# Optimization experiments

Hardware: AMD Instinct MI355X
Metric: run time of the kernel (lower is better)

Reference implementation:

```python
import jax, jax.numpy as jnp
import numpy as np

N_NODES = 50000
N_EDGES = 600000
D = 128
H_MLP = 256
N_LABELS = 10
EPS = 0.0  # tf_geometric GIN default eps


def _gin_layer(x, src, dst, W, b):
    # gather neighbor (source) features and sum-aggregate into destinations
    msg = x[src]                                   # [E, D] irregular gather
    agg = jax.ops.segment_sum(msg, dst, num_segments=N_NODES)  # [N, D]
    h = (1.0 + EPS) * x + agg                      # GIN sum update
    return jax.nn.relu(h @ W + b)                  # dense transform + relu


def setup_inputs() -> dict:
    key = jax.random.key(0)
    ks = jax.random.split(key, 8)
    x = jax.random.normal(ks[0], (N_NODES, D), dtype=jnp.float32)
    edge_index = jax.random.randint(ks[1], (2, N_EDGES), 0, N_NODES, dtype=jnp.int32)
    s = 1.0 / np.sqrt(D)
    W0 = jax.random.normal(ks[2], (D, D), dtype=jnp.float32) * s
    W1 = jax.random.normal(ks[3], (D, D), dtype=jnp.float32) * s
    W2 = jax.random.normal(ks[4], (D, D), dtype=jnp.float32) * s
    Wm1 = jax.random.normal(ks[5], (D, H_MLP), dtype=jnp.float32) * s
    Wm2 = jax.random.normal(ks[6], (H_MLP, N_LABELS), dtype=jnp.float32) * (1.0 / np.sqrt(H_MLP))
    return {
        'x': x, 'edge_index': edge_index,
        'W0': W0, 'b0': jnp.zeros((D,), jnp.float32),
        'W1': W1, 'b1': jnp.zeros((D,), jnp.float32),
        'W2': W2, 'b2': jnp.zeros((D,), jnp.float32),
        'Wm1': Wm1, 'bm1': jnp.zeros((H_MLP,), jnp.float32),
        'Wm2': Wm2, 'bm2': jnp.zeros((N_LABELS,), jnp.float32),
    }


def reference(x, edge_index, W0, b0, W1, b1, W2, b2, Wm1, bm1, Wm2, bm2):
    src, dst = edge_index[0], edge_index[1]
    h = _gin_layer(x, src, dst, W0, b0)
    h = _gin_layer(h, src, dst, W1, b1)
    h = _gin_layer(h, src, dst, W2, b2)
    # head: Flatten is identity on [N, D]; Dense(256, relu) -> Dense(num_labels)
    h = jax.nn.relu(h @ Wm1 + bm1)
    return h @ Wm2 + bm2  # [N, num_labels] logits
```

## Files before the change

kernel.cpp:

```cpp
#include <hip/hip_runtime.h>


typedef short short8 __attribute__((ext_vector_type(8)));
typedef float v4f __attribute__((ext_vector_type(4)));
typedef float v2f __attribute__((ext_vector_type(2)));

#define BCAP 1024
#define MAXB 1024

__device__ inline unsigned short f2bf(float f) {
  union { float f; unsigned int u; } c; c.f = f;
  unsigned int u = c.u;
  return (unsigned short)((u + 0x7fffu + ((u >> 16) & 1u)) >> 16);
}
__device__ inline float bfbits2f(unsigned int hi) {
  union { unsigned int u; float f; } c; c.u = hi; return c.f;
}
__device__ inline unsigned int pack2(float a, float b) {
  return (unsigned int)f2bf(a) | ((unsigned int)f2bf(b) << 16);
}
__device__ inline void add8(float* s, uint4 v) {
  s[0] += bfbits2f(v.x << 16); s[1] += bfbits2f(v.x & 0xffff0000u);
  s[2] += bfbits2f(v.y << 16); s[3] += bfbits2f(v.y & 0xffff0000u);
  s[4] += bfbits2f(v.z << 16); s[5] += bfbits2f(v.z & 0xffff0000u);
  s[6] += bfbits2f(v.w << 16); s[7] += bfbits2f(v.w & 0xffff0000u);
}
__device__ inline void addf8q(float* s, uint4 v) {
  v2f p;
  p = __builtin_amdgcn_cvt_pk_f32_fp8(v.x, false); s[0]  += p.x; s[1]  += p.y;
  p = __builtin_amdgcn_cvt_pk_f32_fp8(v.x, true);  s[2]  += p.x; s[3]  += p.y;
  p = __builtin_amdgcn_cvt_pk_f32_fp8(v.y, false); s[4]  += p.x; s[5]  += p.y;
  p = __builtin_amdgcn_cvt_pk_f32_fp8(v.y, true);  s[6]  += p.x; s[7]  += p.y;
  p = __builtin_amdgcn_cvt_pk_f32_fp8(v.z, false); s[8]  += p.x; s[9]  += p.y;
  p = __builtin_amdgcn_cvt_pk_f32_fp8(v.z, true);  s[10] += p.x; s[11] += p.y;
  p = __builtin_amdgcn_cvt_pk_f32_fp8(v.w, false); s[12] += p.x; s[13] += p.y;
  p = __builtin_amdgcn_cvt_pk_f32_fp8(v.w, true);  s[14] += p.x; s[15] += p.y;
}
__device__ inline unsigned char f2fp8(float v) {
  return (unsigned char)(__builtin_amdgcn_cvt_pk_fp8_f32(v, v, 0, false) & 0xff);
}
__device__ inline int wave_incl_scan_int(int v, int lane) {
#pragma unroll
  for (int off = 1; off < 64; off <<= 1) {
    int t = __shfl_up(v, off, 64);
    if (lane >= off) v += t;
  }
  return v;
}

__global__ __launch_bounds__(256) void prep_all(
    const float* __restrict__ W0, const float* __restrict__ W1, const float* __restrict__ W2,
    const float* __restrict__ Wm1, const float* __restrict__ Wm2,
    unsigned short* __restrict__ W0T, unsigned short* __restrict__ W1T,
    unsigned short* __restrict__ W2T, unsigned short* __restrict__ Wm1T,
    unsigned short* __restrict__ Wm2T,
    const float* __restrict__ x, unsigned short* __restrict__ xb,
    unsigned char* __restrict__ xq, int n8,
    int* __restrict__ bcnt) {
  int i = blockIdx.x * 256 + threadIdx.x;
  if (i < MAXB) bcnt[i] = 0;
  if (i < n8) {
    const float4* p = (const float4*)x;
    float4 a = p[2 * (size_t)i], b = p[2 * (size_t)i + 1];
    uint4 o;
    o.x = pack2(a.x, a.y); o.y = pack2(a.z, a.w);
    o.z = pack2(b.x, b.y); o.w = pack2(b.z, b.w);
    ((uint4*)xb)[i] = o;
    unsigned int lo = 0, hi = 0;
    lo = __builtin_amdgcn_cvt_pk_fp8_f32(a.x, a.y, lo, false);
    lo = __builtin_amdgcn_cvt_pk_fp8_f32(a.z, a.w, lo, true);
    hi = __builtin_amdgcn_cvt_pk_fp8_f32(b.x, b.y, hi, false);
    hi = __builtin_amdgcn_cvt_pk_fp8_f32(b.z, b.w, hi, true);
    uint2 q; q.x = lo; q.y = hi;
    ((uint2*)xq)[i] = q;
  }
  if (i < 49152) {
    int w = i / 16384, r = i % 16384;
    int nn = r >> 7, k = r & 127;
    const float* W = (w == 0) ? W0 : (w == 1) ? W1 : W2;
    unsigned short* O = (w == 0) ? W0T : (w == 1) ? W1T : W2T;
    O[r] = f2bf(W[k * 128 + nn]);
  } else if (i < 49152 + 32768) {
    int r = i - 49152;
    int nn = r >> 7, k = r & 127;
    Wm1T[r] = f2bf(Wm1[k * 256 + nn]);
  } else if (i < 49152 + 32768 + 4096) {
    int r = i - 49152 - 32768;
    int nn = r >> 8, k = r & 255;
    Wm2T[r] = (nn < 10) ? f2bf(Wm2[k * 10 + nn]) : (unsigned short)0;
  }
}

__global__ __launch_bounds__(256) void bin_edges(
    const int* __restrict__ src, const int* __restrict__ dst, int E, int per,
    int* __restrict__ bcnt, int* __restrict__ bucketA, int nbuckets) {
  __shared__ int hist[MAXB];
  __shared__ int base[MAXB];
  const int tid = threadIdx.x;
  const int e0 = blockIdx.x * per;
  const int e1 = (e0 + per < E) ? e0 + per : E;
  for (int j = tid; j < nbuckets; j += 256) hist[j] = 0;
  __syncthreads();
  for (int i = e0 + tid; i < e1; i += 256) atomicAdd(&hist[dst[i] >> 6], 1);
  __syncthreads();
  for (int j = tid; j < nbuckets; j += 256) {
    int h = hist[j];
    base[j] = h ? atomicAdd(&bcnt[j], h) : 0;
  }
  __syncthreads();
  for (int i = e0 + tid; i < e1; i += 256) {
    int d = dst[i], s = src[i];
    int b = d >> 6;
    int r = atomicAdd(&base[b], 1);
    bucketA[(size_t)b * BCAP + r] = (s << 6) | (d & 63);
  }
}

__global__ __launch_bounds__(256) void sort_buckets(
    const int* __restrict__ bcnt, const int* __restrict__ bucketA,
    int* __restrict__ srcsS, int* __restrict__ boffs) {
  __shared__ int rawE[BCAP];
  __shared__ int hist[64], cur[64], offs[65];
  const int tid = threadIdx.x;
  const int b = blockIdx.x;
  const int cnt = bcnt[b];
  for (int i = tid; i < cnt; i += 256) rawE[i] = bucketA[(size_t)b * BCAP + i];
  if (tid < 64) hist[tid] = 0;
  __syncthreads();
  for (int i = tid; i < cnt; i += 256) atomicAdd(&hist[rawE[i] & 63], 1);
  __syncthreads();
  if (tid < 64) {
    int v = hist[tid];
    int incl = wave_incl_scan_int(v, tid);
    offs[tid] = incl - v;
    cur[tid] = incl - v;
    if (tid == 63) offs[64] = incl;
  }
  __syncthreads();
  for (int i = tid; i < cnt; i += 256) {
    int e = rawE[i];
    int p = atomicAdd(&cur[e & 63], 1);
    srcsS[(size_t)b * BCAP + p] = e >> 6;
  }
  if (tid < 65) boffs[b * 65 + tid] = offs[tid];
}

__global__ __launch_bounds__(256) void fused_layer(
    const unsigned short* __restrict__ X, const unsigned char* __restrict__ Xq,
    const int* __restrict__ bcnt,
    const int* __restrict__ srcsS, const int* __restrict__ boffs,
    const unsigned short* __restrict__ BT, const float* __restrict__ bias,
    unsigned short* __restrict__ C, unsigned char* __restrict__ Cq, int M) {
  __shared__ __align__(16) unsigned short As[64 * 136];
  __shared__ int srcS[BCAP];
  __shared__ int offs[65];
  const int tid = threadIdx.x;
  const int lane = tid & 63;
  const int b = blockIdx.x;
  const int blk = b * 64;
  const int cnt = bcnt[b];

  if (tid < 65) offs[tid] = boffs[b * 65 + tid];
  for (int i = tid; i < cnt; i += 256) srcS[i] = srcsS[(size_t)b * BCAP + i];
  __syncthreads();

  const int l = tid & 7, g = tid >> 3;
  const uint4* base = (const uint4*)X;
  const uint4* baseq = (const uint4*)Xq;
#pragma unroll
  for (int s2 = 0; s2 < 2; ++s2) {
    int nl = s2 * 32 + g;
    int node = blk + nl;
    float s[16] = {0, 0, 0, 0, 0, 0, 0, 0, 0, 0, 0, 0, 0, 0, 0, 0};
    if (node < M) {
      add8(s, base[(size_t)node * 16 + l * 2]);
      add8(s + 8, base[(size_t)node * 16 + l * 2 + 1]);
      int beg = offs[nl], c = offs[nl + 1] - beg;
      int j = 0;
      for (; j + 8 <= c; j += 8) {
        int i0 = srcS[beg + j + 0], i1 = srcS[beg + j + 1];
        int i2 = srcS[beg + j + 2], i3 = srcS[beg + j + 3];
        int i4 = srcS[beg + j + 4], i5 = srcS[beg + j + 5];
        int i6 = srcS[beg + j + 6], i7 = srcS[beg + j + 7];
        uint4 v0 = baseq[(size_t)i0 * 8 + l];
        uint4 v1 = baseq[(size_t)i1 * 8 + l];
        uint4 v2 = baseq[(size_t)i2 * 8 + l];
        uint4 v3 = baseq[(size_t)i3 * 8 + l];
        uint4 v4 = baseq[(size_t)i4 * 8 + l];
        uint4 v5 = baseq[(size_t)i5 * 8 + l];
        uint4 v6 = baseq[(size_t)i6 * 8 + l];
        uint4 v7 = baseq[(size_t)i7 * 8 + l];
        addf8q(s, v0); addf8q(s, v1); addf8q(s, v2); addf8q(s, v3);
        addf8q(s, v4); addf8q(s, v5); addf8q(s, v6); addf8q(s, v7);
      }
      if (j + 4 <= c) {
        int i0 = srcS[beg + j + 0], i1 = srcS[beg + j + 1];
        int i2 = srcS[beg + j + 2], i3 = srcS[beg + j + 3];
        uint4 v0 = baseq[(size_t)i0 * 8 + l];
        uint4 v1 = baseq[(size_t)i1 * 8 + l];
        uint4 v2 = baseq[(size_t)i2 * 8 + l];
        uint4 v3 = baseq[(size_t)i3 * 8 + l];
        addf8q(s, v0); addf8q(s, v1); addf8q(s, v2); addf8q(s, v3);
        j += 4;
      }
      if (j + 2 <= c) {
        int i0 = srcS[beg + j + 0], i1 = srcS[beg + j + 1];
        uint4 v0 = baseq[(size_t)i0 * 8 + l];
        uint4 v1 = baseq[(size_t)i1 * 8 + l];
        addf8q(s, v0); addf8q(s, v1);
        j += 2;
      }
      if (j < c) addf8q(s, baseq[(size_t)srcS[beg + j] * 8 + l]);
    }
    uint4 o0, o1;
    o0.x = pack2(s[0], s[1]);   o0.y = pack2(s[2], s[3]);
    o0.z = pack2(s[4], s[5]);   o0.w = pack2(s[6], s[7]);
    o1.x = pack2(s[8], s[9]);   o1.y = pack2(s[10], s[11]);
    o1.z = pack2(s[12], s[13]); o1.w = pack2(s[14], s[15]);
    *(uint4*)&As[nl * 136 + l * 16] = o0;
    *(uint4*)&As[nl * 136 + l * 16 + 8] = o1;
  }
  __syncthreads();

  const int w = tid >> 6;
  const int wm = w & 1, wn = w >> 1;
  const int l15 = lane & 15, quad = lane >> 4;
  const int mb = wm * 32, nb2 = wn * 64;

  const unsigned short* bp[4];
#pragma unroll
  for (int nf = 0; nf < 4; ++nf)
    bp[nf] = BT + (size_t)(nb2 + nf * 16 + l15) * 128 + quad * 8;

  v4f acc[2][4];
#pragma unroll
  for (int mf = 0; mf < 2; ++mf)
#pragma unroll
    for (int nf = 0; nf < 4; ++nf) acc[mf][nf] = (v4f)0.f;

#pragma unroll
  for (int k0 = 0; k0 < 128; k0 += 32) {
    short8 a[2], bv[4];
#pragma unroll
    for (int mf = 0; mf < 2; ++mf)
      a[mf] = *(const short8*)&As[(mb + mf * 16 + l15) * 136 + k0 + quad * 8];
#pragma unroll
    for (int nf = 0; nf < 4; ++nf) bv[nf] = *(const short8*)(bp[nf] + k0);
#pragma unroll
    for (int mf = 0; mf < 2; ++mf)
#pragma unroll
      for (int nf = 0; nf < 4; ++nf)
        acc[mf][nf] = __builtin_amdgcn_mfma_f32_16x16x32_bf16(a[mf], bv[nf], acc[mf][nf], 0, 0, 0);
  }

#pragma unroll
  for (int mf = 0; mf < 2; ++mf) {
#pragma unroll
    for (int r = 0; r < 4; ++r) {
      int grow = blk + mb + mf * 16 + quad * 4 + r;
      if (grow >= M) continue;
#pragma unroll
      for (int nf = 0; nf < 4; ++nf) {
        int gcol = nb2 + nf * 16 + l15;
        float v = fmaxf(acc[mf][nf][r] + bias[gcol], 0.f);
        C[(size_t)grow * 128 + gcol] = f2bf(v);
        Cq[(size_t)grow * 128 + gcol] = f2fp8(v);
      }
    }
  }
}

__global__ __launch_bounds__(256) void fused_l3_head(
    const unsigned short* __restrict__ X, const unsigned char* __restrict__ Xq,
    const int* __restrict__ bcnt,
    const int* __restrict__ srcsS, const int* __restrict__ boffs,
    const unsigned short* __restrict__ W2T, const float* __restrict__ b2,
    const unsigned short* __restrict__ Wm1T, const float* __restrict__ bm1,
    const unsigned short* __restrict__ Wm2T, const float* __restrict__ bm2,
    float* __restrict__ out, int M, int NOUT) {
  __shared__ __align__(16) unsigned char lds[64 * 264 * 2];
  unsigned short* As = (unsigned short*)lds;
  int* srcS = (int*)(lds + 64 * 136 * 2);
  unsigned short* Hs = (unsigned short*)lds;
  __shared__ int offs[65];
  const int tid = threadIdx.x;
  const int lane = tid & 63;
  const int b = blockIdx.x;
  const int blk = b * 64;
  const int cnt = bcnt[b];

  if (tid < 65) offs[tid] = boffs[b * 65 + tid];
  for (int i = tid; i < cnt; i += 256) srcS[i] = srcsS[(size_t)b * BCAP + i];
  __syncthreads();

  const int l = tid & 7, g = tid >> 3;
  const uint4* base = (const uint4*)X;
  const uint4* baseq = (const uint4*)Xq;
#pragma unroll
  for (int s2 = 0; s2 < 2; ++s2) {
    int nl = s2 * 32 + g;
    int node = blk + nl;
    float s[16] = {0, 0, 0, 0, 0, 0, 0, 0, 0, 0, 0, 0, 0, 0, 0, 0};
    if (node < M) {
      add8(s, base[(size_t)node * 16 + l * 2]);
      add8(s + 8, base[(size_t)node * 16 + l * 2 + 1]);
      int beg = offs[nl], c = offs[nl + 1] - beg;
      int j = 0;
      for (; j + 8 <= c; j += 8) {
        int i0 = srcS[beg + j + 0], i1 = srcS[beg + j + 1];
        int i2 = srcS[beg + j + 2], i3 = srcS[beg + j + 3];
        int i4 = srcS[beg + j + 4], i5 = srcS[beg + j + 5];
        int i6 = srcS[beg + j + 6], i7 = srcS[beg + j + 7];
        uint4 v0 = baseq[(size_t)i0 * 8 + l];
        uint4 v1 = baseq[(size_t)i1 * 8 + l];
        uint4 v2 = baseq[(size_t)i2 * 8 + l];
        uint4 v3 = baseq[(size_t)i3 * 8 + l];
        uint4 v4 = baseq[(size_t)i4 * 8 + l];
        uint4 v5 = baseq[(size_t)i5 * 8 + l];
        uint4 v6 = baseq[(size_t)i6 * 8 + l];
        uint4 v7 = baseq[(size_t)i7 * 8 + l];
        addf8q(s, v0); addf8q(s, v1); addf8q(s, v2); addf8q(s, v3);
        addf8q(s, v4); addf8q(s, v5); addf8q(s, v6); addf8q(s, v7);
      }
      if (j + 4 <= c) {
        int i0 = srcS[beg + j + 0], i1 = srcS[beg + j + 1];
        int i2 = srcS[beg + j + 2], i3 = srcS[beg + j + 3];
        uint4 v0 = baseq[(size_t)i0 * 8 + l];
        uint4 v1 = baseq[(size_t)i1 * 8 + l];
        uint4 v2 = baseq[(size_t)i2 * 8 + l];
        uint4 v3 = baseq[(size_t)i3 * 8 + l];
        addf8q(s, v0); addf8q(s, v1); addf8q(s, v2); addf8q(s, v3);
        j += 4;
      }
      if (j + 2 <= c) {
        int i0 = srcS[beg + j + 0], i1 = srcS[beg + j + 1];
        uint4 v0 = baseq[(size_t)i0 * 8 + l];
        uint4 v1 = baseq[(size_t)i1 * 8 + l];
        addf8q(s, v0); addf8q(s, v1);
        j += 2;
      }
      if (j < c) addf8q(s, baseq[(size_t)srcS[beg + j] * 8 + l]);
    }
    uint4 o0, o1;
    o0.x = pack2(s[0], s[1]);   o0.y = pack2(s[2], s[3]);
    o0.z = pack2(s[4], s[5]);   o0.w = pack2(s[6], s[7]);
    o1.x = pack2(s[8], s[9]);   o1.y = pack2(s[10], s[11]);
    o1.z = pack2(s[12], s[13]); o1.w = pack2(s[14], s[15]);
    *(uint4*)&As[nl * 136 + l * 16] = o0;
    *(uint4*)&As[nl * 136 + l * 16 + 8] = o1;
  }
  __syncthreads();

  const int w = tid >> 6;
  const int wm = w & 1, wn = w >> 1;
  const int l15 = lane & 15, quad = lane >> 4;
  const int mb = wm * 32, nb2 = wn * 64;

  v4f acc[2][4];
#pragma unroll
  for (int mf = 0; mf < 2; ++mf)
#pragma unroll
    for (int nf = 0; nf < 4; ++nf) acc[mf][nf] = (v4f)0.f;

#pragma unroll
  for (int k0 = 0; k0 < 128; k0 += 32) {
    short8 a[2], bv[4];
#pragma unroll
    for (int mf = 0; mf < 2; ++mf)
      a[mf] = *(const short8*)&As[(mb + mf * 16 + l15) * 136 + k0 + quad * 8];
#pragma unroll
    for (int nf = 0; nf < 4; ++nf)
      bv[nf] = *(const short8*)(W2T + (size_t)(nb2 + nf * 16 + l15) * 128 + quad * 8 + k0);
#pragma unroll
    for (int mf = 0; mf < 2; ++mf)
#pragma unroll
      for (int nf = 0; nf < 4; ++nf)
        acc[mf][nf] = __builtin_amdgcn_mfma_f32_16x16x32_bf16(a[mf], bv[nf], acc[mf][nf], 0, 0, 0);
  }
  __syncthreads();

#pragma unroll
  for (int mf = 0; mf < 2; ++mf)
#pragma unroll
    for (int r = 0; r < 4; ++r) {
      int row = mb + mf * 16 + quad * 4 + r;
#pragma unroll
      for (int nf = 0; nf < 4; ++nf) {
        int col = nb2 + nf * 16 + l15;
        As[row * 136 + col] = f2bf(fmaxf(acc[mf][nf][r] + b2[col], 0.f));
      }
    }
  __syncthreads();

  const int nbH = wn * 128;
  v4f acc2[2][8];
#pragma unroll
  for (int mf = 0; mf < 2; ++mf)
#pragma unroll
    for (int nf = 0; nf < 8; ++nf) acc2[mf][nf] = (v4f)0.f;

#pragma unroll
  for (int k0 = 0; k0 < 128; k0 += 32) {
    short8 a[2];
#pragma unroll
    for (int mf = 0; mf < 2; ++mf)
      a[mf] = *(const short8*)&As[(mb + mf * 16 + l15) * 136 + k0 + quad * 8];
#pragma unroll
    for (int nf = 0; nf < 8; ++nf) {
      short8 bb = *(const short8*)(Wm1T + (size_t)(nbH + nf * 16 + l15) * 128 + quad * 8 + k0);
#pragma unroll
      for (int mf = 0; mf < 2; ++mf)
        acc2[mf][nf] = __builtin_amdgcn_mfma_f32_16x16x32_bf16(a[mf], bb, acc2[mf][nf], 0, 0, 0);
    }
  }
  __syncthreads();

#pragma unroll
  for (int mf = 0; mf < 2; ++mf)
#pragma unroll
    for (int r = 0; r < 4; ++r) {
      int row = mb + mf * 16 + quad * 4 + r;
#pragma unroll
      for (int nf = 0; nf < 8; ++nf) {
        int col = nbH + nf * 16 + l15;
        Hs[row * 264 + col] = f2bf(fmaxf(acc2[mf][nf][r] + bm1[col], 0.f));
      }
    }
  __syncthreads();

  const int rowl = w * 16 + l15;
  const unsigned short* bp2 = Wm2T + (size_t)l15 * 256 + quad * 8;
  v4f acc3 = (v4f)0.f;
#pragma unroll
  for (int k0 = 0; k0 < 256; k0 += 32)
    acc3 = __builtin_amdgcn_mfma_f32_16x16x32_bf16(
        *(const short8*)&Hs[rowl * 264 + k0 + quad * 8],
        *(const short8*)(bp2 + k0), acc3, 0, 0, 0);
  float bb = (l15 < NOUT) ? bm2[l15] : 0.f;
#pragma unroll
  for (int r = 0; r < 4; ++r) {
    int grow = blk + w * 16 + quad * 4 + r;
    if (grow < M && l15 < NOUT) out[(size_t)grow * NOUT + l15] = acc3[r] + bb;
  }
}


extern "C" void kernel_launch(void* const* d_in, const int* in_sizes, int n_in,
                              void* d_out, int out_size, void* d_ws, size_t ws_size,
                              hipStream_t stream) {
  const float* x   = (const float*)d_in[0];
  const int*   ei  = (const int*)d_in[1];
  const float* W0  = (const float*)d_in[2];
  const float* b0  = (const float*)d_in[3];
  const float* W1  = (const float*)d_in[4];
  const float* b1  = (const float*)d_in[5];
  const float* W2  = (const float*)d_in[6];
  const float* b2  = (const float*)d_in[7];
  const float* Wm1 = (const float*)d_in[8];
  const float* bm1 = (const float*)d_in[9];
  const float* Wm2 = (const float*)d_in[10];
  const float* bm2 = (const float*)d_in[11];
  float* out = (float*)d_out;

  const int D = 128;
  const int N = in_sizes[0] / D;
  const int E = in_sizes[1] / 2;
  const int L = in_sizes[11];
  const int nb = (N + 63) / 64;

  const int* srcv = ei;
  const int* dstv = ei + E;

  char* ws = (char*)d_ws;
  size_t off = 0;
  auto alloc = [&](size_t bytes) -> void* {
    void* p = ws + off;
    off = (off + bytes + 255) & ~(size_t)255;
    return p;
  };
  int* bcnt    = (int*)alloc((size_t)MAXB * 4);
  int* bucketA = (int*)alloc((size_t)nb * BCAP * 4);
  int* srcsS   = (int*)alloc((size_t)nb * BCAP * 4);
  int* boffs   = (int*)alloc((size_t)nb * 65 * 4);
  unsigned short* xb   = (unsigned short*)alloc((size_t)N * 128 * 2);
  unsigned short* h1   = (unsigned short*)alloc((size_t)N * 128 * 2);
  unsigned short* h2   = (unsigned short*)alloc((size_t)N * 128 * 2);
  unsigned char*  xq   = (unsigned char*)alloc((size_t)N * 128);
  unsigned char*  h1q  = (unsigned char*)alloc((size_t)N * 128);
  unsigned char*  h2q  = (unsigned char*)alloc((size_t)N * 128);
  unsigned short* W0T  = (unsigned short*)alloc(128 * 128 * 2);
  unsigned short* W1T  = (unsigned short*)alloc(128 * 128 * 2);
  unsigned short* W2T  = (unsigned short*)alloc(128 * 128 * 2);
  unsigned short* Wm1T = (unsigned short*)alloc(256 * 128 * 2);
  unsigned short* Wm2T = (unsigned short*)alloc(16 * 256 * 2);
  (void)ws_size; (void)n_in; (void)out_size;

  const int tpb = 256;
  int n8 = N * 16;
  prep_all<<<dim3((n8 + tpb - 1) / tpb), dim3(tpb), 0, stream>>>(
      W0, W1, W2, Wm1, Wm2, W0T, W1T, W2T, Wm1T, Wm2T, x, xb, xq, n8, bcnt);

  const int nbin = 256;
  int per = (E + nbin - 1) / nbin;
  bin_edges<<<dim3(nbin), dim3(tpb), 0, stream>>>(srcv, dstv, E, per, bcnt, bucketA, nb);
  sort_buckets<<<dim3(nb), dim3(tpb), 0, stream>>>(bcnt, bucketA, srcsS, boffs);

  dim3 lgrid(nb);
  fused_layer<<<lgrid, dim3(tpb), 0, stream>>>(xb, xq, bcnt, srcsS, boffs, W0T, b0, h1, h1q, N);
  fused_layer<<<lgrid, dim3(tpb), 0, stream>>>(h1, h1q, bcnt, srcsS, boffs, W1T, b1, h2, h2q, N);
  fused_l3_head<<<lgrid, dim3(tpb), 0, stream>>>(h2, h2q, bcnt, srcsS, boffs, W2T, b2,
                                                 Wm1T, bm1, Wm2T, bm2, out, N, L);
}
```

Measured before the change: 224.9 us.

## Drop bf16 hidden copies, read self features from fp8, stage Wm1 in LDS

Layers 1 and 2 now write only the fp8 copy of their output, and later layers read the self term from that fp8 buffer, so the bf16 h1/h2 writes and reads go away. The head kernel copies Wm1T into padded dynamic shared memory (about 101 KB total) instead of reading it from global memory inside the MFMA loop. The trade-off is lower precision on the self term and much lower occupancy for the head kernel, since the larger LDS footprint allows roughly one block per CU.

After: 239.7 us. 1.07x slower.

```diff
diff --git a/kernel.cpp b/kernel.cpp
--- a/kernel.cpp
+++ b/kernel.cpp
@@ -7,6 +7,7 @@
 
 #define BCAP 1024
 #define MAXB 1024
+#define L3_DYN 103424
 
 __device__ inline unsigned short f2bf(float f) {
   union { float f; unsigned int u; } c; c.f = f;
@@ -146,11 +147,11 @@
 }
 
 __global__ __launch_bounds__(256) void fused_layer(
-    const unsigned short* __restrict__ X, const unsigned char* __restrict__ Xq,
+    const unsigned short* __restrict__ Xb, const unsigned char* __restrict__ Xq,
     const int* __restrict__ bcnt,
     const int* __restrict__ srcsS, const int* __restrict__ boffs,
     const unsigned short* __restrict__ BT, const float* __restrict__ bias,
-    unsigned short* __restrict__ C, unsigned char* __restrict__ Cq, int M) {
+    unsigned char* __restrict__ Cq, int M) {
   __shared__ __align__(16) unsigned short As[64 * 136];
   __shared__ int srcS[BCAP];
   __shared__ int offs[65];
@@ -165,7 +166,7 @@
   __syncthreads();
 
   const int l = tid & 7, g = tid >> 3;
-  const uint4* base = (const uint4*)X;
+  const uint4* baseb = (const uint4*)Xb;
   const uint4* baseq = (const uint4*)Xq;
 #pragma unroll
   for (int s2 = 0; s2 < 2; ++s2) {
@@ -173,8 +174,12 @@
     int node = blk + nl;
     float s[16] = {0, 0, 0, 0, 0, 0, 0, 0, 0, 0, 0, 0, 0, 0, 0, 0};
     if (node < M) {
-      add8(s, base[(size_t)node * 16 + l * 2]);
-      add8(s + 8, base[(size_t)node * 16 + l * 2 + 1]);
+      if (Xb) {
+        add8(s, baseb[(size_t)node * 16 + l * 2]);
+        add8(s + 8, baseb[(size_t)node * 16 + l * 2 + 1]);
+      } else {
+        addf8q(s, baseq[(size_t)node * 8 + l]);
+      }
       int beg = offs[nl], c = offs[nl + 1] - beg;
       int j = 0;
       for (; j + 8 <= c; j += 8) {
@@ -263,7 +268,6 @@
       for (int nf = 0; nf < 4; ++nf) {
         int gcol = nb2 + nf * 16 + l15;
         float v = fmaxf(acc[mf][nf][r] + bias[gcol], 0.f);
-        C[(size_t)grow * 128 + gcol] = f2bf(v);
         Cq[(size_t)grow * 128 + gcol] = f2fp8(v);
       }
     }
@@ -271,17 +275,19 @@
 }
 
 __global__ __launch_bounds__(256) void fused_l3_head(
-    const unsigned short* __restrict__ X, const unsigned char* __restrict__ Xq,
+    const unsigned char* __restrict__ Xq,
     const int* __restrict__ bcnt,
     const int* __restrict__ srcsS, const int* __restrict__ boffs,
     const unsigned short* __restrict__ W2T, const float* __restrict__ b2,
     const unsigned short* __restrict__ Wm1T, const float* __restrict__ bm1,
     const unsigned short* __restrict__ Wm2T, const float* __restrict__ bm2,
     float* __restrict__ out, int M, int NOUT) {
-  __shared__ __align__(16) unsigned char lds[64 * 264 * 2];
-  unsigned short* As = (unsigned short*)lds;
-  int* srcS = (int*)(lds + 64 * 136 * 2);
-  unsigned short* Hs = (unsigned short*)lds;
+  extern __shared__ __align__(16) char dyn[];
+  unsigned short* Wm1L = (unsigned short*)dyn;
+  char* U = dyn + 69632;
+  unsigned short* As = (unsigned short*)U;
+  int* srcS = (int*)(U + 64 * 136 * 2);
+  unsigned short* Hs = (unsigned short*)U;
   __shared__ int offs[65];
   const int tid = threadIdx.x;
   const int lane = tid & 63;
@@ -291,10 +297,13 @@
 
   if (tid < 65) offs[tid] = boffs[b * 65 + tid];
   for (int i = tid; i < cnt; i += 256) srcS[i] = srcsS[(size_t)b * BCAP + i];
+  for (int c = tid; c < 4096; c += 256) {
+    int row = c >> 4, ch = c & 15;
+    *(uint4*)&Wm1L[row * 136 + ch * 8] = *(const uint4*)&Wm1T[row * 128 + ch * 8];
+  }
   __syncthreads();
 
   const int l = tid & 7, g = tid >> 3;
-  const uint4* base = (const uint4*)X;
   const uint4* baseq = (const uint4*)Xq;
 #pragma unroll
   for (int s2 = 0; s2 < 2; ++s2) {
@@ -302,8 +311,7 @@
     int node = blk + nl;
     float s[16] = {0, 0, 0, 0, 0, 0, 0, 0, 0, 0, 0, 0, 0, 0, 0, 0};
     if (node < M) {
-      add8(s, base[(size_t)node * 16 + l * 2]);
-      add8(s + 8, base[(size_t)node * 16 + l * 2 + 1]);
+      addf8q(s, baseq[(size_t)node * 8 + l]);
       int beg = offs[nl], c = offs[nl + 1] - beg;
       int j = 0;
       for (; j + 8 <= c; j += 8) {
@@ -407,7 +415,7 @@
       a[mf] = *(const short8*)&As[(mb + mf * 16 + l15) * 136 + k0 + quad * 8];
 #pragma unroll
     for (int nf = 0; nf < 8; ++nf) {
-      short8 bb = *(const short8*)(Wm1T + (size_t)(nbH + nf * 16 + l15) * 128 + quad * 8 + k0);
+      short8 bb = *(const short8*)&Wm1L[(nbH + nf * 16 + l15) * 136 + quad * 8 + k0];
 #pragma unroll
       for (int mf = 0; mf < 2; ++mf)
         acc2[mf][nf] = __builtin_amdgcn_mfma_f32_16x16x32_bf16(a[mf], bb, acc2[mf][nf], 0, 0, 0);
@@ -483,8 +491,6 @@
   int* srcsS   = (int*)alloc((size_t)nb * BCAP * 4);
   int* boffs   = (int*)alloc((size_t)nb * 65 * 4);
   unsigned short* xb   = (unsigned short*)alloc((size_t)N * 128 * 2);
-  unsigned short* h1   = (unsigned short*)alloc((size_t)N * 128 * 2);
-  unsigned short* h2   = (unsigned short*)alloc((size_t)N * 128 * 2);
   unsigned char*  xq   = (unsigned char*)alloc((size_t)N * 128);
   unsigned char*  h1q  = (unsigned char*)alloc((size_t)N * 128);
   unsigned char*  h2q  = (unsigned char*)alloc((size_t)N * 128);
@@ -495,6 +501,13 @@
   unsigned short* Wm2T = (unsigned short*)alloc(16 * 256 * 2);
   (void)ws_size; (void)n_in; (void)out_size;
 
+  static bool attr_done = false;
+  if (!attr_done) {
+    hipFuncSetAttribute(reinterpret_cast<const void*>(fused_l3_head),
+                        hipFuncAttributeMaxDynamicSharedMemorySize, L3_DYN);
+    attr_done = true;
+  }
+
   const int tpb = 256;
   int n8 = N * 16;
   prep_all<<<dim3((n8 + tpb - 1) / tpb), dim3(tpb), 0, stream>>>(
@@ -506,8 +519,10 @@
   sort_buckets<<<dim3(nb), dim3(tpb), 0, stream>>>(bcnt, bucketA, srcsS, boffs);
 
   dim3 lgrid(nb);
-  fused_layer<<<lgrid, dim3(tpb), 0, stream>>>(xb, xq, bcnt, srcsS, boffs, W0T, b0, h1, h1q, N);
-  fused_layer<<<lgrid, dim3(tpb), 0, stream>>>(h1, h1q, bcnt, srcsS, boffs, W1T, b1, h2, h2q, N);
-  fused_l3_head<<<lgrid, dim3(tpb), 0, stream>>>(h2, h2q, bcnt, srcsS, boffs, W2T, b2,
-                                                 Wm1T, bm1, Wm2T, bm2, out, N, L);
-}
+  fused_layer<<<lgrid, dim3(tpb), 0, stream>>>(
+      xb, xq, bcnt, srcsS, boffs, W0T, b0, h1q, N);
+  fused_layer<<<lgrid, dim3(tpb), 0, stream>>>(
+      nullptr, h1q, bcnt, srcsS, boffs, W1T, b1, h2q, N);
+  fused_l3_head<<<lgrid, dim3(tpb), L3_DYN, stream>>>(
+      h2q, bcnt, srcsS, boffs, W2T, b2, Wm1T, bm1, Wm2T, bm2, out, N, L);
+}
```
